# Kernel tuning notes

Hardware: AMD Instinct MI355X
Metric: run time of the kernel (lower is better)

Reference implementation:

```python
import jax, jax.numpy as jnp
import numpy as np

EPS = 1e-5  # torch BatchNorm2d default


def _signature_depth3(path):
    """Truncated (depth-3) path signature via Chen's relation.
    path: [B, P, ch] (P points). Returns [B, ch + ch^2 + ch^3] in signatory
    layout (level 1, then row-major flattened levels 2 and 3)."""
    dx = path[:, 1:] - path[:, :-1]  # [B, P-1, ch] increments
    B, _, ch = dx.shape

    def step(carry, v):
        s1, s2, s3 = carry  # [B,ch], [B,ch,ch], [B,ch,ch,ch]
        vv = v[:, :, None] * v[:, None, :]          # v (x) v
        e2 = 0.5 * vv                               # v^(x)2 / 2!
        e3 = vv[:, :, :, None] * v[:, None, None, :] / 6.0  # v^(x)3 / 3!
        n1 = s1 + v
        n2 = s2 + s1[:, :, None] * v[:, None, :] + e2
        n3 = (s3
              + s2[:, :, :, None] * v[:, None, None, :]
              + s1[:, :, None, None] * e2[:, None, :, :]
              + e3)
        return (n1, n2, n3), None

    init = (jnp.zeros((B, ch), dx.dtype),
            jnp.zeros((B, ch, ch), dx.dtype),
            jnp.zeros((B, ch, ch, ch), dx.dtype))
    (s1, s2, s3), _ = jax.lax.scan(step, init, jnp.transpose(dx, (1, 0, 2)))
    return jnp.concatenate([s1, s2.reshape(B, -1), s3.reshape(B, -1)], axis=1)


def setup_inputs() -> dict:
    key = jax.random.key(0)
    ks = jax.random.split(key, 5)
    N, C, J, T, L = 16, 64, 25, 128, 9
    sic, out_dim = 8, 64
    ch = sic + 1                      # +1 time channel
    sig_ch = ch + ch**2 + ch**3       # 819
    x = jax.random.normal(ks[0], (N, C, J, T, L), jnp.float32)
    conv_w = jax.random.normal(ks[1], (sic, C), jnp.float32) * 0.1
    conv_b = jax.random.normal(ks[2], (sic,), jnp.float32) * 0.1
    bn_gamma = jnp.ones((sic,), jnp.float32)
    bn_beta = jnp.zeros((sic,), jnp.float32)
    lin_w = jax.random.normal(ks[3], (out_dim, sig_ch), jnp.float32) * 0.03
    lin_b = jax.random.normal(ks[4], (out_dim,), jnp.float32) * 0.03
    return dict(x=x, conv_w=conv_w, conv_b=conv_b, bn_gamma=bn_gamma,
                bn_beta=bn_beta, lin_w=lin_w, lin_b=lin_b)


def reference(x, conv_w, conv_b, bn_gamma, bn_beta, lin_w, lin_b):
    N, C, J, T, L = x.shape
    # 1x1 conv over channel dim (applied to [N*L, C, J, T] in torch, which is
    # the same per-position linear map)
    y = jnp.einsum('ncjtl,oc->nojtl', x, conv_w) + conv_b[None, :, None, None, None]
    y = jax.nn.relu(y)
    # BatchNorm2d (training mode): stats over all dims except channel
    mean = y.mean(axis=(0, 2, 3, 4), keepdims=True)
    var = ((y - mean) ** 2).mean(axis=(0, 2, 3, 4), keepdims=True)
    y = ((y - mean) * jax.lax.rsqrt(var + EPS)
         * bn_gamma[None, :, None, None, None] + bn_beta[None, :, None, None, None])
    # -> [N*J*T, L, sic] stream per (n, joint, frame)
    B = N * J * T
    p = jnp.transpose(y, (0, 2, 3, 4, 1)).reshape(B, L, -1)
    # signatory.Augment(include_time=True): prepend time channel in [0, 1]
    t = jnp.broadcast_to(jnp.linspace(0.0, 1.0, L, dtype=x.dtype)[None, :, None], (B, L, 1))
    p = jnp.concatenate([t, p], axis=-1)  # [B, L, ch]
    # signature(..., basepoint=True): prepend zero point
    path = jnp.concatenate([jnp.zeros((B, 1, p.shape[-1]), p.dtype), p], axis=1)
    sig = _signature_depth3(path)          # [B, 819]
    z = sig @ lin_w.T + lin_b              # [B, out_dim]
    return jnp.transpose(z.reshape(N, J, T, -1), (0, 3, 1, 2))  # [N, C, J, T]
```

## Files before the change

kernel.cpp:

```cpp
#include <hip/hip_runtime.h>
#include <hip/hip_bf16.h>

typedef unsigned short u16;
typedef __attribute__((ext_vector_type(8))) short short8;
typedef __attribute__((ext_vector_type(4))) float f32x4;

#define N_    16
#define C_    64
#define J_    25
#define T_    128
#define L_    9
#define SIC   8
#define OUT_  64
#define BTOT  (N_*J_*T_)
#define CNT   (BTOT*L_)
#define KPAD  896
#define NKS   27
#define SPB   28

#define K1C_BLOCKS 900
#define K1BT_BLOCKS 224
#define BT_ELEMS (OUT_*KPAD)

#define PART_OFF  0
#define SS_OFF    16384
#define BT_OFF    32768
#define Y_OFF     65536
#define WS_NEED   ((size_t)(Y_OFF + BTOT*72) * 4)

__device__ __forceinline__ short to_bf16(float x) {
  union { __hip_bfloat16 h; u16 u; } cv;
  cv.h = __float2bfloat16(x);
  return (short)cv.u;
}

__global__ __launch_bounds__(256) void k1_conv(
    const float* __restrict__ x, const float* __restrict__ cw,
    const float* __restrict__ cb, const float* __restrict__ lw,
    float* __restrict__ yws, float* __restrict__ part, u16* __restrict__ Bt) {
  int tid = threadIdx.x;

  if (blockIdx.x >= K1C_BLOCKS) {
    int idx = (blockIdx.x - K1C_BLOCKS) * 256 + tid;
    if (idx < BT_ELEMS) {
      int o = idx / KPAD, k = idx % KPAD;
      float v = 0.f;
      if (k < 864) {
        int i = k / 96, p = k % 96;
        if (p < 91) {
          int orig = (p == 0) ? i : (p < 10 ? 9 + i * 9 + (p - 1) : 90 + i * 81 + (p - 10));
          v = lw[o * 819 + orig];
        }
      }
      Bt[idx] = (u16)to_bf16(v);
    }
    return;
  }

  __shared__ float wlT[C_ * SIC];
  __shared__ float bl[SIC];
  __shared__ float wsum[4][16];
  wlT[tid] = cw[(tid & 7) * C_ + (tid >> 3)];
  wlT[tid + 256] = cw[(tid & 7) * C_ + ((tid + 256) >> 3)];
  if (tid < SIC) bl[tid] = cb[tid];
  __syncthreads();

  int p0 = (blockIdx.x * 256 + tid) * 2;
  int n = p0 / 28800, rem = p0 % 28800;
  int jj = rem / 1152, tl0 = rem % 1152;
  const float* xp = x + (size_t)(n * 1600 + jj) * 1152 + tl0;

  float acc[2][8];
#pragma unroll
  for (int p = 0; p < 2; p++)
#pragma unroll
    for (int o = 0; o < 8; o++) acc[p][o] = bl[o];

#pragma unroll 8
  for (int c = 0; c < C_; c++) {
    float2 xv = *(const float2*)(xp + (size_t)c * 28800);
    float4 w0 = *(const float4*)&wlT[c * 8];
    float4 w1 = *(const float4*)&wlT[c * 8 + 4];
    acc[0][0] = fmaf(xv.x, w0.x, acc[0][0]); acc[1][0] = fmaf(xv.y, w0.x, acc[1][0]);
    acc[0][1] = fmaf(xv.x, w0.y, acc[0][1]); acc[1][1] = fmaf(xv.y, w0.y, acc[1][1]);
    acc[0][2] = fmaf(xv.x, w0.z, acc[0][2]); acc[1][2] = fmaf(xv.y, w0.z, acc[1][2]);
    acc[0][3] = fmaf(xv.x, w0.w, acc[0][3]); acc[1][3] = fmaf(xv.y, w0.w, acc[1][3]);
    acc[0][4] = fmaf(xv.x, w1.x, acc[0][4]); acc[1][4] = fmaf(xv.y, w1.x, acc[1][4]);
    acc[0][5] = fmaf(xv.x, w1.y, acc[0][5]); acc[1][5] = fmaf(xv.y, w1.y, acc[1][5]);
    acc[0][6] = fmaf(xv.x, w1.z, acc[0][6]); acc[1][6] = fmaf(xv.y, w1.z, acc[1][6]);
    acc[0][7] = fmaf(xv.x, w1.w, acc[0][7]); acc[1][7] = fmaf(xv.y, w1.w, acc[1][7]);
  }

  float vals[16];
#pragma unroll
  for (int q = 0; q < 16; q++) vals[q] = 0.f;
  float4* dst = (float4*)(yws + (size_t)p0 * 8);
#pragma unroll
  for (int p = 0; p < 2; p++) {
#pragma unroll
    for (int o = 0; o < 8; o++) acc[p][o] = fmaxf(acc[p][o], 0.f);
    dst[p * 2]     = make_float4(acc[p][0], acc[p][1], acc[p][2], acc[p][3]);
    dst[p * 2 + 1] = make_float4(acc[p][4], acc[p][5], acc[p][6], acc[p][7]);
#pragma unroll
    for (int o = 0; o < 8; o++) {
      vals[o] += acc[p][o];
      vals[8 + o] += acc[p][o] * acc[p][o];
    }
  }

  int lane = tid & 63, wid = tid >> 6;
#pragma unroll
  for (int v = 0; v < 16; v++) {
    float s = vals[v];
    for (int off = 32; off > 0; off >>= 1) s += __shfl_down(s, off, 64);
    if (lane == 0) wsum[wid][v] = s;
  }
  __syncthreads();
  if (tid < 16)
    part[blockIdx.x * 16 + tid] = wsum[0][tid] + wsum[1][tid] + wsum[2][tid] + wsum[3][tid];
}

__global__ __launch_bounds__(256) void k2_stats(
    const float* __restrict__ part, const float* __restrict__ gamma,
    const float* __restrict__ beta, float* __restrict__ ss) {
  __shared__ float red[16][16];
  int tid = threadIdx.x;
  int val = tid & 15, grp = tid >> 4;
  float s0 = 0.f, s1 = 0.f, s2 = 0.f, s3 = 0.f;
  int b = grp;
  for (; b + 48 < K1C_BLOCKS; b += 64) {
    s0 += part[b * 16 + val];
    s1 += part[(b + 16) * 16 + val];
    s2 += part[(b + 32) * 16 + val];
    s3 += part[(b + 48) * 16 + val];
  }
  for (; b < K1C_BLOCKS; b += 16) s0 += part[b * 16 + val];
  red[grp][val] = (s0 + s1) + (s2 + s3);
  __syncthreads();
  if (tid < 16) {
    float tot = 0.f;
#pragma unroll
    for (int g = 0; g < 16; g++) tot += red[g][tid];
    red[0][tid] = tot;
  }
  __syncthreads();
  if (tid < 8) {
    float mean = red[0][tid] * (1.f / CNT);
    float var  = red[0][8 + tid] * (1.f / CNT) - mean * mean;
    float sc = gamma[tid] * rsqrtf(var + 1e-5f);
    ss[tid] = sc;
    ss[8 + tid] = beta[tid] - mean * sc;
  }
}

#define SIG_STEP(vi_)                                                       \
  do {                                                                      \
    float aa = fmaf((vi_), (1.f / 6.f), 0.5f * s1);                         \
    float b2 = fmaf((vi_), 0.5f, s1);                                       \
    _Pragma("unroll")                                                       \
    for (int jj = 0; jj < 9; jj++) {                                        \
      float tj = fmaf(aa, v[jj], s2[jj]);                                   \
      _Pragma("unroll")                                                     \
      for (int kk = 0; kk < 9; kk++)                                        \
        s3[jj * 9 + kk] = fmaf(tj, v[kk], s3[jj * 9 + kk]);                 \
      s2[jj] = fmaf(b2, v[jj], s2[jj]);                                     \
    }                                                                       \
    s1 += (vi_);                                                            \
  } while (0)

__global__ __launch_bounds__(256, 3) void k3_fused(
    const float* __restrict__ yws, const float* __restrict__ ss,
    const u16* __restrict__ Bt, const float* __restrict__ lb,
    float* __restrict__ out) {
  __shared__ __align__(16) u16 sig_lds[29 * KPAD];
  __shared__ float ssl[16];
  __shared__ float lbl[64];
  float* ylds = (float*)sig_lds;
  int tid = threadIdx.x;
  int gBase = blockIdx.x * SPB;
  int valid = BTOT - gBase; if (valid > SPB) valid = SPB;

  int sA = tid / 9;
  bool actA = (tid < SPB * 9) && (sA < valid);
  float4 ya = make_float4(0.f, 0.f, 0.f, 0.f), yb = ya;
  if (actA) {
    const float4* src = (const float4*)(yws + (size_t)gBase * 72 + (size_t)tid * 8);
    ya = src[0]; yb = src[1];
  }
  if (tid < 16) ssl[tid] = ss[tid];
  if (tid >= 64 && tid < 128) lbl[tid - 64] = lb[tid - 64];
  {
    short8 z = {0, 0, 0, 0, 0, 0, 0, 0};
    int padChunks = (29 - valid) * 112;
    for (int e = tid; e < padChunks; e += 256) {
      int r = valid + e / 112, sl = e % 112;
      *(short8*)&sig_lds[r * KPAD + sl * 8] = z;
    }
  }
  __syncthreads();

  if (actA) {
    float* drow = ylds + tid * 8;
    drow[0] = fmaf(ya.x, ssl[0], ssl[8]);
    drow[1] = fmaf(ya.y, ssl[1], ssl[9]);
    drow[2] = fmaf(ya.z, ssl[2], ssl[10]);
    drow[3] = fmaf(ya.w, ssl[3], ssl[11]);
    drow[4] = fmaf(yb.x, ssl[4], ssl[12]);
    drow[5] = fmaf(yb.y, ssl[5], ssl[13]);
    drow[6] = fmaf(yb.z, ssl[6], ssl[14]);
    drow[7] = fmaf(yb.w, ssl[7], ssl[15]);
  }
  __syncthreads();

  int s = tid / 9, i = tid % 9;
  bool act = actA;
  float s1 = 0.f, s2[9], s3[81];
#pragma unroll
  for (int jj = 0; jj < 9; jj++) s2[jj] = 0.f;
#pragma unroll
  for (int q = 0; q < 81; q++) s3[q] = 0.f;
  if (act) {
    const float* yrow = ylds + s * 72;
    int i1 = (i == 0) ? 0 : (i - 1);
    float prevvi;
    {
      float4 a4 = *(const float4*)(yrow);
      float4 b4 = *(const float4*)(yrow + 4);
      float v[9] = {0.f, a4.x, a4.y, a4.z, a4.w, b4.x, b4.y, b4.z, b4.w};
      float curvi = (i == 0) ? 0.f : yrow[i1];
      SIG_STEP(curvi);
      prevvi = curvi;
    }
#pragma unroll 1
    for (int l = 1; l < 9; l++) {
      float4 a4 = *(const float4*)(yrow + l * 8);
      float4 b4 = *(const float4*)(yrow + l * 8 + 4);
      float4 p4 = *(const float4*)(yrow + (l - 1) * 8);
      float4 q4 = *(const float4*)(yrow + (l - 1) * 8 + 4);
      float v[9];
      v[0] = 0.125f;
      v[1] = a4.x - p4.x; v[2] = a4.y - p4.y; v[3] = a4.z - p4.z; v[4] = a4.w - p4.w;
      v[5] = b4.x - q4.x; v[6] = b4.y - q4.y; v[7] = b4.z - q4.z; v[8] = b4.w - q4.w;
      float curvi = (i == 0) ? (float)l * 0.125f : yrow[l * 8 + i1];
      float vi = curvi - prevvi;
      prevvi = curvi;
      SIG_STEP(vi);
    }
  }
  __syncthreads();

  if (act) {
    u16* rowbase = sig_lds + s * KPAD;
    int sw = s & 7;
    {
      short8 ch;
      ch[0] = to_bf16(s1);
#pragma unroll
      for (int w = 0; w < 7; w++) ch[w + 1] = to_bf16(s2[w]);
      *(short8*)&rowbase[(((i * 12 + 0) ^ sw) * 8)] = ch;
    }
    {
      short8 ch;
      ch[0] = to_bf16(s2[7]); ch[1] = to_bf16(s2[8]);
#pragma unroll
      for (int w = 0; w < 6; w++) ch[w + 2] = to_bf16(s3[w]);
      *(short8*)&rowbase[(((i * 12 + 1) ^ sw) * 8)] = ch;
    }
#pragma unroll
    for (int c = 2; c <= 10; c++) {
      short8 ch;
#pragma unroll
      for (int w = 0; w < 8; w++) ch[w] = to_bf16(s3[c * 8 - 10 + w]);
      *(short8*)&rowbase[(((i * 12 + c) ^ sw) * 8)] = ch;
    }
    {
      short8 ch;
      ch[0] = to_bf16(s3[78]); ch[1] = to_bf16(s3[79]); ch[2] = to_bf16(s3[80]);
      ch[3] = 0; ch[4] = 0; ch[5] = 0; ch[6] = 0; ch[7] = 0;
      *(short8*)&rowbase[(((i * 12 + 11) ^ sw) * 8)] = ch;
    }
  }

  int w = tid >> 6, l = tid & 63;
  int brow = (w << 4) + (l & 15);
  const short8* bp = (const short8*)(Bt + (size_t)brow * KPAD);
  int s4base = (l >> 4);
  int arow0 = (l & 15);
  int arow1 = 16 + (l & 15); if (arow1 > 28) arow1 = 28;
  int asw0 = arow0 & 7, asw1 = arow1 & 7;
  short8 bcur = bp[s4base];
  __syncthreads();

  short8 a0c = *(const short8*)&sig_lds[arow0 * KPAD + ((s4base ^ asw0) * 8)];
  short8 a1c = *(const short8*)&sig_lds[arow1 * KPAD + ((s4base ^ asw1) * 8)];
  f32x4 acc0 = {0, 0, 0, 0}, acc1 = {0, 0, 0, 0};
#pragma unroll
  for (int ks = 0; ks < NKS; ks++) {
    short8 bn, a0n, a1n;
    if (ks + 1 < NKS) {
      int s4n = (ks + 1) * 4 + s4base;
      bn  = bp[s4n];
      a0n = *(const short8*)&sig_lds[arow0 * KPAD + ((s4n ^ asw0) * 8)];
      a1n = *(const short8*)&sig_lds[arow1 * KPAD + ((s4n ^ asw1) * 8)];
    }
    acc0 = __builtin_amdgcn_mfma_f32_16x16x32_bf16(a0c, bcur, acc0, 0, 0, 0);
    acc1 = __builtin_amdgcn_mfma_f32_16x16x32_bf16(a1c, bcur, acc1, 0, 0, 0);
    if (ks + 1 < NKS) { bcur = bn; a0c = a0n; a1c = a1n; }
  }
  __syncthreads();

  float* c_lds = (float*)sig_lds;
  int o = (w << 4) + (l & 15);
#pragma unroll
  for (int r = 0; r < 4; r++) {
    int m0 = (l >> 4) * 4 + r;
    c_lds[o * 33 + m0] = acc0[r];
    c_lds[o * 33 + 16 + m0] = acc1[r];
  }
  __syncthreads();
  for (int e = tid; e < 2048; e += 256) {
    int o2 = e >> 5, m = e & 31;
    if (m < valid) {
      int b = gBase + m;
      int n = b / (J_ * T_), rem = b % (J_ * T_);
      int j = rem >> 7, t = rem & (T_ - 1);
      out[(((size_t)n * OUT_ + o2) * J_ + j) * T_ + t] = c_lds[o2 * 33 + m] + lbl[o2];
    }
  }
}

extern "C" void kernel_launch(void* const* d_in, const int* in_sizes, int n_in,
                              void* d_out, int out_size, void* d_ws, size_t ws_size,
                              hipStream_t stream) {
  const float* x     = (const float*)d_in[0];
  const float* cw    = (const float*)d_in[1];
  const float* cb    = (const float*)d_in[2];
  const float* gamma = (const float*)d_in[3];
  const float* beta  = (const float*)d_in[4];
  const float* lw    = (const float*)d_in[5];
  const float* lbias = (const float*)d_in[6];
  float* out = (float*)d_out;
  float* ws  = (float*)d_ws;
  if (ws_size < WS_NEED) return;

  float* part = ws + PART_OFF;
  float* ss   = ws + SS_OFF;
  u16*   bt   = (u16*)(ws + BT_OFF);
  float* yws  = ws + Y_OFF;

  hipLaunchKernelGGL(k1_conv, dim3(K1C_BLOCKS + K1BT_BLOCKS), dim3(256), 0, stream,
                     x, cw, cb, lw, yws, part, bt);
  hipLaunchKernelGGL(k2_stats, dim3(1), dim3(256), 0, stream, part, gamma, beta, ss);

  int nblk3 = (BTOT + SPB - 1) / SPB;
  hipLaunchKernelGGL(k3_fused, dim3(nblk3), dim3(256), 0, stream, yws, ss, bt, lbias, out);
}
```

Measured before the change: 70.52 us.

## Fold BatchNorm stats reduction into fused kernel and double-prefetch B operand

Removes the single-block stats kernel and has every block of the fused kernel redundantly reduce the 900x16 partial sums itself using vector loads and wave shuffles, then compute the scale and shift in shared memory. This drops one kernel launch and its serial dependency, at the cost of each of roughly 1800 blocks re-reading about 57KB of partials, which should mostly hit cache. The MFMA loop also prefetches the global B operand two steps ahead instead of one to hide load latency.

```diff
diff --git a/kernel.cpp b/kernel.cpp
--- a/kernel.cpp
+++ b/kernel.cpp
@@ -21,9 +21,9 @@
 #define K1C_BLOCKS 900
 #define K1BT_BLOCKS 224
 #define BT_ELEMS (OUT_*KPAD)
+#define PART_F4  (K1C_BLOCKS*4)
 
 #define PART_OFF  0
-#define SS_OFF    16384
 #define BT_OFF    32768
 #define Y_OFF     65536
 #define WS_NEED   ((size_t)(Y_OFF + BTOT*72) * 4)
@@ -118,39 +118,6 @@
   __syncthreads();
   if (tid < 16)
     part[blockIdx.x * 16 + tid] = wsum[0][tid] + wsum[1][tid] + wsum[2][tid] + wsum[3][tid];
-}
-
-__global__ __launch_bounds__(256) void k2_stats(
-    const float* __restrict__ part, const float* __restrict__ gamma,
-    const float* __restrict__ beta, float* __restrict__ ss) {
-  __shared__ float red[16][16];
-  int tid = threadIdx.x;
-  int val = tid & 15, grp = tid >> 4;
-  float s0 = 0.f, s1 = 0.f, s2 = 0.f, s3 = 0.f;
-  int b = grp;
-  for (; b + 48 < K1C_BLOCKS; b += 64) {
-    s0 += part[b * 16 + val];
-    s1 += part[(b + 16) * 16 + val];
-    s2 += part[(b + 32) * 16 + val];
-    s3 += part[(b + 48) * 16 + val];
-  }
-  for (; b < K1C_BLOCKS; b += 16) s0 += part[b * 16 + val];
-  red[grp][val] = (s0 + s1) + (s2 + s3);
-  __syncthreads();
-  if (tid < 16) {
-    float tot = 0.f;
-#pragma unroll
-    for (int g = 0; g < 16; g++) tot += red[g][tid];
-    red[0][tid] = tot;
-  }
-  __syncthreads();
-  if (tid < 8) {
-    float mean = red[0][tid] * (1.f / CNT);
-    float var  = red[0][8 + tid] * (1.f / CNT) - mean * mean;
-    float sc = gamma[tid] * rsqrtf(var + 1e-5f);
-    ss[tid] = sc;
-    ss[8 + tid] = beta[tid] - mean * sc;
-  }
 }
 
 #define SIG_STEP(vi_)                                                       \
@@ -169,12 +136,15 @@
   } while (0)
 
 __global__ __launch_bounds__(256, 3) void k3_fused(
-    const float* __restrict__ yws, const float* __restrict__ ss,
+    const float* __restrict__ yws, const float* __restrict__ part,
+    const float* __restrict__ gamma, const float* __restrict__ beta,
     const u16* __restrict__ Bt, const float* __restrict__ lb,
     float* __restrict__ out) {
   __shared__ __align__(16) u16 sig_lds[29 * KPAD];
   __shared__ float ssl[16];
   __shared__ float lbl[64];
+  __shared__ float red4[4][4][4];
+  __shared__ float sarr[16];
   float* ylds = (float*)sig_lds;
   int tid = threadIdx.x;
   int gBase = blockIdx.x * SPB;
@@ -187,8 +157,25 @@
     const float4* src = (const float4*)(yws + (size_t)gBase * 72 + (size_t)tid * 8);
     ya = src[0]; yb = src[1];
   }
-  if (tid < 16) ssl[tid] = ss[tid];
+  float gm = 0.f, bt_ = 0.f;
+  if (tid < 8) { gm = gamma[tid]; bt_ = beta[tid]; }
   if (tid >= 64 && tid < 128) lbl[tid - 64] = lb[tid - 64];
+
+  f32x4 pacc = {0.f, 0.f, 0.f, 0.f};
+  for (int q = tid; q < PART_F4; q += 256) {
+    f32x4 v = *(const f32x4*)(part + (size_t)q * 4);
+    pacc += v;
+  }
+  int lane = tid & 63, wid = tid >> 6;
+#pragma unroll
+  for (int off = 32; off >= 4; off >>= 1) {
+#pragma unroll
+    for (int c = 0; c < 4; c++) pacc[c] += __shfl_down(pacc[c], off, 64);
+  }
+  if (lane < 4) {
+#pragma unroll
+    for (int c = 0; c < 4; c++) red4[wid][lane][c] = pacc[c];
+  }
   {
     short8 z = {0, 0, 0, 0, 0, 0, 0, 0};
     int padChunks = (29 - valid) * 112;
@@ -196,6 +183,20 @@
       int r = valid + e / 112, sl = e % 112;
       *(short8*)&sig_lds[r * KPAD + sl * 8] = z;
     }
+  }
+  __syncthreads();
+  if (tid < 16) {
+    int cg = tid >> 2, comp = tid & 3;
+    sarr[tid] = (red4[0][cg][comp] + red4[1][cg][comp])
+              + (red4[2][cg][comp] + red4[3][cg][comp]);
+  }
+  __syncthreads();
+  if (tid < 8) {
+    float mean = sarr[tid] * (1.f / CNT);
+    float var  = sarr[8 + tid] * (1.f / CNT) - mean * mean;
+    float sc = gm * rsqrtf(var + 1e-5f);
+    ssl[tid] = sc;
+    ssl[8 + tid] = bt_ - mean * sc;
   }
   __syncthreads();
 
@@ -288,24 +289,25 @@
   int arow0 = (l & 15);
   int arow1 = 16 + (l & 15); if (arow1 > 28) arow1 = 28;
   int asw0 = arow0 & 7, asw1 = arow1 & 7;
-  short8 bcur = bp[s4base];
-  __syncthreads();
+  short8 bq0 = bp[s4base];
+  __syncthreads();
+  short8 bq1 = bp[4 + s4base];
 
   short8 a0c = *(const short8*)&sig_lds[arow0 * KPAD + ((s4base ^ asw0) * 8)];
   short8 a1c = *(const short8*)&sig_lds[arow1 * KPAD + ((s4base ^ asw1) * 8)];
   f32x4 acc0 = {0, 0, 0, 0}, acc1 = {0, 0, 0, 0};
 #pragma unroll
   for (int ks = 0; ks < NKS; ks++) {
-    short8 bn, a0n, a1n;
+    short8 bn = bq1, a0n = a0c, a1n = a1c;
+    if (ks + 2 < NKS) bn = bp[(ks + 2) * 4 + s4base];
     if (ks + 1 < NKS) {
       int s4n = (ks + 1) * 4 + s4base;
-      bn  = bp[s4n];
       a0n = *(const short8*)&sig_lds[arow0 * KPAD + ((s4n ^ asw0) * 8)];
       a1n = *(const short8*)&sig_lds[arow1 * KPAD + ((s4n ^ asw1) * 8)];
     }
-    acc0 = __builtin_amdgcn_mfma_f32_16x16x32_bf16(a0c, bcur, acc0, 0, 0, 0);
-    acc1 = __builtin_amdgcn_mfma_f32_16x16x32_bf16(a1c, bcur, acc1, 0, 0, 0);
-    if (ks + 1 < NKS) { bcur = bn; a0c = a0n; a1c = a1n; }
+    acc0 = __builtin_amdgcn_mfma_f32_16x16x32_bf16(a0c, bq0, acc0, 0, 0, 0);
+    acc1 = __builtin_amdgcn_mfma_f32_16x16x32_bf16(a1c, bq0, acc1, 0, 0, 0);
+    bq0 = bq1; bq1 = bn; a0c = a0n; a1c = a1n;
   }
   __syncthreads();
 
@@ -344,14 +346,13 @@
   if (ws_size < WS_NEED) return;
 
   float* part = ws + PART_OFF;
-  float* ss   = ws + SS_OFF;
   u16*   bt   = (u16*)(ws + BT_OFF);
   float* yws  = ws + Y_OFF;
 
   hipLaunchKernelGGL(k1_conv, dim3(K1C_BLOCKS + K1BT_BLOCKS), dim3(256), 0, stream,
                      x, cw, cb, lw, yws, part, bt);
-  hipLaunchKernelGGL(k2_stats, dim3(1), dim3(256), 0, stream, part, gamma, beta, ss);
 
   int nblk3 = (BTOT + SPB - 1) / SPB;
-  hipLaunchKernelGGL(k3_fused, dim3(nblk3), dim3(256), 0, stream, yws, ss, bt, lbias, out);
+  hipLaunchKernelGGL(k3_fused, dim3(nblk3), dim3(256), 0, stream,
+                     yws, part, gamma, beta, bt, lbias, out);
 }
```

Result: slower. 77.49 us (+9.9%).
